# Optimization experiments

Measured on AMD Instinct MI355X. Metric: run time of the kernel, lower is better.

## Reference

```python
import jax, jax.numpy as jnp
import numpy as np

N_USERS = 100000
N_ITEMS = 50000
N_NODES = 50000
N_EDGES = 1600000
B = 16384
H, D = 4, 32  # num_heads, out_feats per head
D_IMG, D_TXT, D_AUD = 1024, 768, 128
EMB = 128
SLOPE = 0.2


def setup_inputs() -> dict:
    key = jax.random.key(0)
    ks = jax.random.split(key, 40)
    s = 0.02

    def n(i, shape, scale=s):
        return jax.random.normal(ks[i], shape, jnp.float32) * scale

    inp = {
        "user_ids": jax.random.randint(ks[0], (B,), 0, N_USERS, jnp.int32),
        "item_ids": jax.random.randint(ks[1], (B,), 0, N_ITEMS, jnp.int32),
        "src": jax.random.randint(ks[2], (N_EDGES,), 0, N_NODES, jnp.int32),
        "dst": jax.random.randint(ks[3], (N_EDGES,), 0, N_NODES, jnp.int32),
        "feat_image": jax.random.normal(ks[4], (N_NODES, D_IMG), jnp.float32),
        "feat_text": jax.random.normal(ks[5], (N_NODES, D_TXT), jnp.float32),
        "feat_audio": jax.random.normal(ks[6], (N_NODES, D_AUD), jnp.float32),
        # embedding tables
        "user_table": n(7, (N_USERS, EMB)),
        "item_table": n(8, (N_ITEMS, EMB)),
        # modality transforms (Linear: y = x @ W.T + b)
        "Wi": n(9, (32, D_IMG)), "bi": n(10, (32,)),
        "Wt": n(11, (32, D_TXT)), "bt": n(12, (32,)),
        "Wa": n(13, (32, D_AUD)), "ba": n(14, (32,)),
        # GAT params per modality: fc weight [H*D, 32], attn vectors [H, D], output bias [H*D]
        "gWi": n(15, (H * D, 32), 0.1), "ali": n(16, (H, D), 0.1), "ari": n(17, (H, D), 0.1), "gbi": n(18, (H * D,)),
        "gWt": n(19, (H * D, 32), 0.1), "alt": n(20, (H, D), 0.1), "art": n(21, (H, D), 0.1), "gbt": n(22, (H * D,)),
        "gWa": n(23, (H * D, 32), 0.1), "ala": n(24, (H, D), 0.1), "ara": n(25, (H, D), 0.1), "gba": n(26, (H * D,)),
        # final fc: Linear(32*3*H=384 -> 128)
        "fcW": n(27, (EMB, 3 * H * D)), "fcb": n(28, (EMB,)),
    }
    return inp


def _gat(x, W, al, ar, b, src, dst):
    """DGL GATConv: fc -> per-head additive attention -> edge softmax over dst -> sum."""
    h = (x @ W.T).reshape(N_NODES, H, D)                      # [N,H,D]
    el = jnp.einsum('nhd,hd->nh', h, al)                      # [N,H]
    er = jnp.einsum('nhd,hd->nh', h, ar)                      # [N,H]
    e = jax.nn.leaky_relu(el[src] + er[dst], SLOPE)           # [E,H]
    emax = jax.ops.segment_max(e, dst, num_segments=N_NODES)  # [N,H] (-inf for empty, unused)
    a = jnp.exp(e - emax[dst])                                # [E,H]
    denom = jax.ops.segment_sum(a, dst, num_segments=N_NODES)
    a = a / jnp.maximum(denom[dst], 1e-9)
    msg = a[:, :, None] * h[src]                              # [E,H,D]
    out = jax.ops.segment_sum(msg, dst, num_segments=N_NODES) # [N,H,D]
    return (out + b.reshape(1, H, D)).reshape(N_NODES, H * D)


def reference(user_ids, item_ids, src, dst, feat_image, feat_text, feat_audio,
              user_table, item_table, Wi, bi, Wt, bt, Wa, ba,
              gWi, ali, ari, gbi, gWt, alt, art, gbt, gWa, ala, ara, gba,
              fcW, fcb):
    user_emb = user_table[user_ids]
    item_emb = item_table[item_ids]
    xi = jax.nn.relu(feat_image @ Wi.T + bi)
    xt = jax.nn.relu(feat_text @ Wt.T + bt)
    xa = jax.nn.relu(feat_audio @ Wa.T + ba)
    gi = _gat(xi, gWi, ali, ari, gbi, src, dst)
    gt = _gat(xt, gWt, alt, art, gbt, src, dst)
    ga = _gat(xa, gWa, ala, ara, gba, src, dst)
    comb = jnp.concatenate([gi, gt, ga], axis=1)              # [N, 3*H*D]
    comb = jax.nn.relu(comb @ fcW.T + fcb)                    # [N, 128]
    return (user_emb, item_emb, comb)
```

## Files before the change

### kernel.cpp

```cpp
#include <hip/hip_runtime.h>
#include <stdint.h>

#define NNODES 50000
#define NEDGES 1600000
#define NB     16384
#define HD     128
#define COMBW  384
#define SCAN_BLOCKS ((NNODES + 255) / 256)

typedef unsigned short u16;
typedef __bf16 bf16x8 __attribute__((ext_vector_type(8)));
typedef float  f32x4  __attribute__((ext_vector_type(4)));

__device__ __forceinline__ float b2f(u16 u){
    union { unsigned int i; float f; } v; v.i = ((unsigned int)u) << 16; return v.f;
}
__device__ __forceinline__ u16 f2b(float f){
    union { float f; unsigned int i; } v; v.f = f;
    unsigned int x = v.i;
    unsigned int r = (x + 0x7fffu + ((x >> 16) & 1u)) >> 16;
    return (u16)r;
}
__device__ __forceinline__ bf16x8 pack8(const float* __restrict__ p){
    uint4 a = *(const uint4*)p;
    uint4 b = *(const uint4*)(p + 4);
    union { u16 s[8]; bf16x8 v; } u;
    u.s[0] = (u16)(a.x >> 16); u.s[1] = (u16)(a.y >> 16);
    u.s[2] = (u16)(a.z >> 16); u.s[3] = (u16)(a.w >> 16);
    u.s[4] = (u16)(b.x >> 16); u.s[5] = (u16)(b.y >> 16);
    u.s[6] = (u16)(b.z >> 16); u.s[7] = (u16)(b.w >> 16);
    return u.v;
}

__global__ void k_gather(const int* __restrict__ uid, const int* __restrict__ iid,
                         const float* __restrict__ utab, const float* __restrict__ itab,
                         float* __restrict__ out){
    int i = blockIdx.x * blockDim.x + threadIdx.x;
    const int total = 2 * NB * HD / 8;
    if (i >= total) return;
    int e8 = i * 8;
    const float* p;
    if (e8 < NB * HD) {
        int row = e8 >> 7, c = e8 & 127;
        p = utab + (size_t)uid[row] * HD + c;
    } else {
        int e2 = e8 - NB * HD;
        int row = e2 >> 7, c = e2 & 127;
        p = itab + (size_t)iid[row] * HD + c;
    }
    *(uint4*)(out + e8)     = *(const uint4*)p;
    *(uint4*)(out + e8 + 4) = *(const uint4*)(p + 4);
}

__global__ __launch_bounds__(256) void k_feat(const float* __restrict__ feat, int K,
                                              const float* __restrict__ W,
                                              const float* __restrict__ bias,
                                              float* __restrict__ xout){
    int wave = threadIdx.x >> 6, lane = threadIdx.x & 63;
    int quad = lane >> 4, m = lane & 15;
    int row0 = blockIdx.x * 64 + wave * 16;
    int arow = row0 + m; if (arow >= NNODES) arow = NNODES - 1;
    const float* ap  = feat + (size_t)arow * K + quad * 8;
    const float* bp0 = W + (size_t)m        * K + quad * 8;
    const float* bp1 = W + (size_t)(m + 16) * K + quad * 8;
    f32x4 c0 = {0.f,0.f,0.f,0.f}, c1 = {0.f,0.f,0.f,0.f};
    for (int k = 0; k < K; k += 32){
        bf16x8 a  = pack8(ap  + k);
        bf16x8 b0 = pack8(bp0 + k);
        bf16x8 b1 = pack8(bp1 + k);
        c0 = __builtin_amdgcn_mfma_f32_16x16x32_bf16(a, b0, c0, 0, 0, 0);
        c1 = __builtin_amdgcn_mfma_f32_16x16x32_bf16(a, b1, c1, 0, 0, 0);
    }
    float bv0 = bias[m], bv1 = bias[m + 16];
    #pragma unroll
    for (int i = 0; i < 4; i++){
        int r = row0 + quad * 4 + i;
        if (r < NNODES){
            float v0 = c0[i] + bv0; v0 = v0 > 0.f ? v0 : 0.f;
            float v1 = c1[i] + bv1; v1 = v1 > 0.f ? v1 : 0.f;
            xout[(size_t)r * 32 + m]      = v0;
            xout[(size_t)r * 32 + m + 16] = v1;
        }
    }
}

__global__ __launch_bounds__(256) void k_node(const float* __restrict__ x,
                                              const float* __restrict__ gW,
                                              const float* __restrict__ al,
                                              const float* __restrict__ ar,
                                              u16* __restrict__ hout,
                                              float* __restrict__ el,
                                              float* __restrict__ er){
    int head = blockIdx.y;
    int n = blockIdx.x * blockDim.x + threadIdx.x;
    int nc = n < NNODES ? n : NNODES - 1;
    float xr[32];
    const float4* xp = (const float4*)(x + (size_t)nc * 32);
    #pragma unroll
    for (int i = 0; i < 8; i++){
        float4 v = xp[i];
        xr[4*i] = v.x; xr[4*i+1] = v.y; xr[4*i+2] = v.z; xr[4*i+3] = v.w;
    }
    const float* wbase = gW + head * 1024;
    const float* alh = al + head * 32;
    const float* arh = ar + head * 32;
    u16* hp = hout + (size_t)nc * COMBW + head * 32;
    float elv = 0.f, erv = 0.f;
    #pragma unroll
    for (int cg = 0; cg < 4; cg++){
        float acc[8];
        #pragma unroll
        for (int c = 0; c < 8; c++){
            const float* wr = wbase + (cg * 8 + c) * 32;
            float a = 0.f;
            #pragma unroll
            for (int k = 0; k < 32; k++) a += xr[k] * wr[k];
            acc[c] = a;
            elv += a * alh[cg * 8 + c];
            erv += a * arh[cg * 8 + c];
        }
        union { u16 s[8]; uint4 q; } u;
        #pragma unroll
        for (int c = 0; c < 8; c++) u.s[c] = f2b(acc[c]);
        *(uint4*)(hp + cg * 8) = u.q;
    }
    el[(size_t)nc * 4 + head] = elv;
    er[(size_t)nc * 4 + head] = erv;
}

__global__ void k_hist(const int* __restrict__ dst, int* __restrict__ cnt){
    int i = blockIdx.x * blockDim.x + threadIdx.x;
    if (i < NEDGES) atomicAdd(&cnt[dst[i]], 1);
}

__global__ __launch_bounds__(256) void k_scan1(const int* __restrict__ cnt,
                                               int* __restrict__ rp,
                                               int* __restrict__ bsum){
    __shared__ int ws[4];
    int t = threadIdx.x, lane = t & 63, w = t >> 6;
    int i = blockIdx.x * 256 + t;
    int v = (i < NNODES) ? cnt[i] : 0;
    int x = v;
    #pragma unroll
    for (int off = 1; off < 64; off <<= 1){
        int u = __shfl_up(x, off, 64);
        if (lane >= off) x += u;
    }
    if (lane == 63) ws[w] = x;
    __syncthreads();
    if (t == 0){
        int s = 0;
        #pragma unroll
        for (int j = 0; j < 4; j++){ int tmp = ws[j]; ws[j] = s; s += tmp; }
        bsum[blockIdx.x] = s;
    }
    __syncthreads();
    if (i < NNODES) rp[i] = ws[w] + x - v;
}

__global__ __launch_bounds__(256) void k_scan2(int* __restrict__ bsum, int* __restrict__ rp){
    __shared__ int ws[4];
    int t = threadIdx.x, lane = t & 63, w = t >> 6;
    int v = (t < SCAN_BLOCKS) ? bsum[t] : 0;
    int x = v;
    #pragma unroll
    for (int off = 1; off < 64; off <<= 1){
        int u = __shfl_up(x, off, 64);
        if (lane >= off) x += u;
    }
    if (lane == 63) ws[w] = x;
    __syncthreads();
    if (t == 0){
        int s = 0;
        #pragma unroll
        for (int j = 0; j < 4; j++){ int tmp = ws[j]; ws[j] = s; s += tmp; }
        rp[NNODES] = s;
    }
    __syncthreads();
    if (t < SCAN_BLOCKS) bsum[t] = ws[w] + x - v;
}

__global__ __launch_bounds__(256) void k_scan3(int* __restrict__ rp, const int* __restrict__ bsum){
    int i = blockIdx.x * 256 + threadIdx.x;
    if (i < NNODES) rp[i] += bsum[blockIdx.x];
}

template<int WITHW>
__global__ __launch_bounds__(256) void k_scatter(const int* __restrict__ src, const int* __restrict__ dst,
                          const int* __restrict__ rp, int* __restrict__ fill,
                          int* __restrict__ col,
                          const float* __restrict__ el0, const float* __restrict__ er0,
                          const float* __restrict__ el1, const float* __restrict__ er1,
                          const float* __restrict__ el2, const float* __restrict__ er2,
                          float* __restrict__ w){
    int i = blockIdx.x * blockDim.x + threadIdx.x;
    if (i >= NEDGES) return;
    int s = src[i], d = dst[i];
    int p = rp[d] + atomicAdd(&fill[d], 1);
    col[p] = s;
    if (WITHW){
        float4 l0 = *(const float4*)(el0 + (size_t)s * 4);
        float4 r0 = *(const float4*)(er0 + (size_t)d * 4);
        float4 l1 = *(const float4*)(el1 + (size_t)s * 4);
        float4 r1 = *(const float4*)(er1 + (size_t)d * 4);
        float4 l2 = *(const float4*)(el2 + (size_t)s * 4);
        float4 r2 = *(const float4*)(er2 + (size_t)d * 4);
        float4 w0, w1, w2;
        #define LKEXP(a, b) __expf(fmaxf((a) + (b), 0.2f * ((a) + (b))))
        w0.x = LKEXP(l0.x, r0.x); w0.y = LKEXP(l0.y, r0.y); w0.z = LKEXP(l0.z, r0.z); w0.w = LKEXP(l0.w, r0.w);
        w1.x = LKEXP(l1.x, r1.x); w1.y = LKEXP(l1.y, r1.y); w1.z = LKEXP(l1.z, r1.z); w1.w = LKEXP(l1.w, r1.w);
        w2.x = LKEXP(l2.x, r2.x); w2.y = LKEXP(l2.y, r2.y); w2.z = LKEXP(l2.z, r2.z); w2.w = LKEXP(l2.w, r2.w);
        #undef LKEXP
        float4* wp = (float4*)(w + (size_t)p * 12);
        wp[0] = w0; wp[1] = w1; wp[2] = w2;
    }
}

__global__ __launch_bounds__(384) void k_gat(
        const int* __restrict__ rp, const int* __restrict__ col,
        const u16* __restrict__ hcat, const float* __restrict__ w,
        const float* __restrict__ gb0, const float* __restrict__ gb1, const float* __restrict__ gb2,
        u16* __restrict__ comb){
    int n = blockIdx.x, t = threadIdx.x;
    int mod = t >> 7;
    int head = (t >> 5) & 3;
    int beg = rp[n], end = rp[n + 1];
    float acc = 0.f, dsum = 0.f;
    const float* wp = w + (size_t)beg * 12 + mod * 4 + head;
    const u16* hbase = hcat + t;
    int e = beg;
    for (; e + 4 <= end; e += 4){
        int s0 = col[e], s1 = col[e + 1], s2 = col[e + 2], s3 = col[e + 3];
        float w0 = wp[0], w1 = wp[12], w2 = wp[24], w3 = wp[36];
        wp += 48;
        float h0 = b2f(hbase[(size_t)s0 * COMBW]);
        float h1 = b2f(hbase[(size_t)s1 * COMBW]);
        float h2 = b2f(hbase[(size_t)s2 * COMBW]);
        float h3 = b2f(hbase[(size_t)s3 * COMBW]);
        acc += w0 * h0; dsum += w0;
        acc += w1 * h1; dsum += w1;
        acc += w2 * h2; dsum += w2;
        acc += w3 * h3; dsum += w3;
    }
    for (; e < end; e++, wp += 12){
        int s = col[e];
        float wv = wp[0];
        acc += wv * b2f(hbase[(size_t)s * COMBW]);
        dsum += wv;
    }
    const float* gb = (mod == 0) ? gb0 : ((mod == 1) ? gb1 : gb2);
    comb[(size_t)n * COMBW + t] = f2b(acc / fmaxf(dsum, 1e-9f) + gb[t & 127]);
}

__global__ __launch_bounds__(128) void k_gat_fb(
        const int* __restrict__ rp, const int* __restrict__ col,
        const u16* __restrict__ hcat,
        const float* __restrict__ el0, const float* __restrict__ er0,
        const float* __restrict__ el1, const float* __restrict__ er1,
        const float* __restrict__ el2, const float* __restrict__ er2,
        const float* __restrict__ gb0, const float* __restrict__ gb1, const float* __restrict__ gb2,
        u16* __restrict__ comb){
    int n = blockIdx.x, t = threadIdx.x;
    int head = t >> 5;
    float a0 = 0.f, a1 = 0.f, a2 = 0.f, d0 = 0.f, d1 = 0.f, d2 = 0.f;
    int beg = rp[n], end = rp[n + 1];
    float e0 = er0[(size_t)n * 4 + head];
    float e1 = er1[(size_t)n * 4 + head];
    float e2 = er2[(size_t)n * 4 + head];
    for (int e = beg; e < end; e++){
        int s = col[e];
        const u16* hp = hcat + (size_t)s * COMBW + t;
        float v0 = el0[(size_t)s * 4 + head] + e0; v0 = fmaxf(v0, 0.2f * v0);
        float v1 = el1[(size_t)s * 4 + head] + e1; v1 = fmaxf(v1, 0.2f * v1);
        float v2 = el2[(size_t)s * 4 + head] + e2; v2 = fmaxf(v2, 0.2f * v2);
        float w0 = __expf(v0), w1 = __expf(v1), w2 = __expf(v2);
        a0 += w0 * b2f(hp[0]);   d0 += w0;
        a1 += w1 * b2f(hp[128]); d1 += w1;
        a2 += w2 * b2f(hp[256]); d2 += w2;
    }
    size_t o = (size_t)n * COMBW;
    comb[o + t]       = f2b(a0 / fmaxf(d0, 1e-9f) + gb0[t]);
    comb[o + 128 + t] = f2b(a1 / fmaxf(d1, 1e-9f) + gb1[t]);
    comb[o + 256 + t] = f2b(a2 / fmaxf(d2, 1e-9f) + gb2[t]);
}

__global__ __launch_bounds__(256) void k_fc(const u16* __restrict__ comb,
                                            const float* __restrict__ fcW,
                                            const float* __restrict__ fcb,
                                            float* __restrict__ out){
    int wave = threadIdx.x >> 6, lane = threadIdx.x & 63;
    int quad = lane >> 4, m = lane & 15;
    int row0 = blockIdx.x * 64 + wave * 16;
    int arow = row0 + m; if (arow >= NNODES) arow = NNODES - 1;
    const u16* ap = comb + (size_t)arow * COMBW + quad * 8;
    f32x4 c[8];
    #pragma unroll
    for (int f = 0; f < 8; f++) c[f] = (f32x4){0.f,0.f,0.f,0.f};
    for (int k = 0; k < COMBW; k += 32){
        bf16x8 a = *(const bf16x8*)(ap + k);
        #pragma unroll
        for (int f = 0; f < 8; f++){
            bf16x8 b = pack8(fcW + (size_t)(f * 16 + m) * COMBW + k + quad * 8);
            c[f] = __builtin_amdgcn_mfma_f32_16x16x32_bf16(a, b, c[f], 0, 0, 0);
        }
    }
    #pragma unroll
    for (int f = 0; f < 8; f++){
        int colc = f * 16 + m;
        float bv = fcb[colc];
        #pragma unroll
        for (int i = 0; i < 4; i++){
            int r = row0 + quad * 4 + i;
            if (r < NNODES){
                float v = c[f][i] + bv; v = v > 0.f ? v : 0.f;
                out[(size_t)(2 * NB * HD) + (size_t)r * HD + colc] = v;
            }
        }
    }
}

extern "C" void kernel_launch(void* const* d_in, const int* in_sizes, int n_in,
                              void* d_out, int out_size, void* d_ws, size_t ws_size,
                              hipStream_t stream){
    const int* uid = (const int*)d_in[0];
    const int* iid = (const int*)d_in[1];
    const int* src = (const int*)d_in[2];
    const int* dst = (const int*)d_in[3];
    const float* fimg = (const float*)d_in[4];
    const float* ftxt = (const float*)d_in[5];
    const float* faud = (const float*)d_in[6];
    const float* utab = (const float*)d_in[7];
    const float* itab = (const float*)d_in[8];
    const float* Wi = (const float*)d_in[9],  *bi = (const float*)d_in[10];
    const float* Wt = (const float*)d_in[11], *bt = (const float*)d_in[12];
    const float* Wa = (const float*)d_in[13], *ba = (const float*)d_in[14];
    const float* gWi = (const float*)d_in[15], *ali = (const float*)d_in[16],
               *ari = (const float*)d_in[17], *gbi = (const float*)d_in[18];
    const float* gWt = (const float*)d_in[19], *alt = (const float*)d_in[20],
               *art = (const float*)d_in[21], *gbt = (const float*)d_in[22];
    const float* gWa = (const float*)d_in[23], *ala = (const float*)d_in[24],
               *ara = (const float*)d_in[25], *gba = (const float*)d_in[26];
    const float* fcW = (const float*)d_in[27], *fcb = (const float*)d_in[28];
    float* out = (float*)d_out;

    char* ws = (char*)d_ws;
    u16*   hcat = (u16*)  (ws + 0);
    u16*   comb = (u16*)  (ws + 38400000);
    float* x    = (float*)(ws + 76800000);
    float* el   = (float*)(ws + 83200000);
    float* er   = (float*)(ws + 85600000);
    int*   cnt  = (int*)  (ws + 88000000);
    int*   fill = (int*)  (ws + 88200000);
    int*   rp   = (int*)  (ws + 88400000);
    int*   col  = (int*)  (ws + 88600064);
    float* w    = (float*)(ws + 95000064);
    const size_t NEED_W = 95000064u + (size_t)NEDGES * 12 * sizeof(float);
    int*   bsum = (int*)x;

    float* el0 = el,           *el1 = el + 200000, *el2 = el + 400000;
    float* er0 = er,           *er1 = er + 200000, *er2 = er + 400000;

    hipMemsetAsync(cnt, 0, 400000, stream);

    k_hist<<<(NEDGES + 255) / 256, 256, 0, stream>>>(dst, cnt);
    k_scan1<<<SCAN_BLOCKS, 256, 0, stream>>>(cnt, rp, bsum);
    k_scan2<<<1, 256, 0, stream>>>(bsum, rp);
    k_scan3<<<SCAN_BLOCKS, 256, 0, stream>>>(rp, bsum);

    k_gather<<<(2 * NB * HD / 8 + 255) / 256, 256, 0, stream>>>(uid, iid, utab, itab, out);

    dim3 ngrid((NNODES + 255) / 256, 4);
    k_feat<<<(NNODES + 63) / 64, 256, 0, stream>>>(fimg, 1024, Wi, bi, x);
    k_node<<<ngrid, 256, 0, stream>>>(x, gWi, ali, ari, hcat,       el0, er0);
    k_feat<<<(NNODES + 63) / 64, 256, 0, stream>>>(ftxt, 768, Wt, bt, x);
    k_node<<<ngrid, 256, 0, stream>>>(x, gWt, alt, art, hcat + 128, el1, er1);
    k_feat<<<(NNODES + 63) / 64, 256, 0, stream>>>(faud, 128, Wa, ba, x);
    k_node<<<ngrid, 256, 0, stream>>>(x, gWa, ala, ara, hcat + 256, el2, er2);

    if (ws_size >= NEED_W){
        k_scatter<1><<<(NEDGES + 255) / 256, 256, 0, stream>>>(src, dst, rp, fill, col,
                                                               el0, er0, el1, er1, el2, er2, w);
        k_gat<<<NNODES, 384, 0, stream>>>(rp, col, hcat, w, gbi, gbt, gba, comb);
    } else {
        k_scatter<0><<<(NEDGES + 255) / 256, 256, 0, stream>>>(src, dst, rp, fill, col,
                                                               el0, er0, el1, er1, el2, er2, w);
        k_gat_fb<<<NNODES, 128, 0, stream>>>(rp, col, hcat,
                                             el0, er0, el1, er1, el2, er2,
                                             gbi, gbt, gba, comb);
    }

    k_fc<<<(NNODES + 63) / 64, 256, 0, stream>>>(comb, fcW, fcb, out);
}
```

Baseline: 1.217 ms.

## Pre-pack weights to bf16 and restructure GAT aggregation to 128 threads per node

Adds small kernels that convert the modality and final fc weight matrices to bf16 once per call, so the MFMA loops in k_feat and k_fc load ready bf16 vectors instead of repacking fp32 weights in every block. The packed weights reuse workspace regions (comb, w) that are free at that point. k_gat now uses 128 threads per node, each handling all three modalities, to raise per-thread memory-level parallelism and cut block count overhead. The risk is lower occupancy per node and slightly different rounding, since packing truncates rather than rounds to nearest.

```diff
diff --git a/kernel.cpp b/kernel.cpp
--- a/kernel.cpp
+++ b/kernel.cpp
@@ -52,22 +52,55 @@
     *(uint4*)(out + e8 + 4) = *(const uint4*)(p + 4);
 }
 
+__global__ __launch_bounds__(256) void k_pack(const float* __restrict__ s,
+                                              u16* __restrict__ d, int n8){
+    int i = blockIdx.x * 256 + threadIdx.x;
+    if (i >= n8) return;
+    const float* p = s + (size_t)i * 8;
+    uint4 a = *(const uint4*)p, b = *(const uint4*)(p + 4);
+    union { u16 v[8]; uint4 q; } u;
+    u.v[0] = (u16)(a.x >> 16); u.v[1] = (u16)(a.y >> 16);
+    u.v[2] = (u16)(a.z >> 16); u.v[3] = (u16)(a.w >> 16);
+    u.v[4] = (u16)(b.x >> 16); u.v[5] = (u16)(b.y >> 16);
+    u.v[6] = (u16)(b.z >> 16); u.v[7] = (u16)(b.w >> 16);
+    *(uint4*)(d + (size_t)i * 8) = u.q;
+}
+
+__global__ __launch_bounds__(256) void k_pack3(const float* __restrict__ Wi,
+                                               const float* __restrict__ Wt,
+                                               const float* __restrict__ Wa,
+                                               u16* __restrict__ d){
+    int i = blockIdx.x * 256 + threadIdx.x;
+    if (i >= 7680) return;
+    const float* p;
+    if (i < 4096)       p = Wi + (size_t)i * 8;
+    else if (i < 7168)  p = Wt + (size_t)(i - 4096) * 8;
+    else                p = Wa + (size_t)(i - 7168) * 8;
+    uint4 a = *(const uint4*)p, b = *(const uint4*)(p + 4);
+    union { u16 v[8]; uint4 q; } u;
+    u.v[0] = (u16)(a.x >> 16); u.v[1] = (u16)(a.y >> 16);
+    u.v[2] = (u16)(a.z >> 16); u.v[3] = (u16)(a.w >> 16);
+    u.v[4] = (u16)(b.x >> 16); u.v[5] = (u16)(b.y >> 16);
+    u.v[6] = (u16)(b.z >> 16); u.v[7] = (u16)(b.w >> 16);
+    *(uint4*)(d + (size_t)i * 8) = u.q;
+}
+
 __global__ __launch_bounds__(256) void k_feat(const float* __restrict__ feat, int K,
-                                              const float* __restrict__ W,
+                                              const u16* __restrict__ pW,
                                               const float* __restrict__ bias,
                                               float* __restrict__ xout){
     int wave = threadIdx.x >> 6, lane = threadIdx.x & 63;
     int quad = lane >> 4, m = lane & 15;
     int row0 = blockIdx.x * 64 + wave * 16;
     int arow = row0 + m; if (arow >= NNODES) arow = NNODES - 1;
-    const float* ap  = feat + (size_t)arow * K + quad * 8;
-    const float* bp0 = W + (size_t)m        * K + quad * 8;
-    const float* bp1 = W + (size_t)(m + 16) * K + quad * 8;
+    const float* ap = feat + (size_t)arow * K + quad * 8;
+    const u16* bp0 = pW + (size_t)m        * K + quad * 8;
+    const u16* bp1 = pW + (size_t)(m + 16) * K + quad * 8;
     f32x4 c0 = {0.f,0.f,0.f,0.f}, c1 = {0.f,0.f,0.f,0.f};
     for (int k = 0; k < K; k += 32){
-        bf16x8 a  = pack8(ap  + k);
-        bf16x8 b0 = pack8(bp0 + k);
-        bf16x8 b1 = pack8(bp1 + k);
+        bf16x8 a  = pack8(ap + k);
+        bf16x8 b0 = *(const bf16x8*)(bp0 + k);
+        bf16x8 b1 = *(const bf16x8*)(bp1 + k);
         c0 = __builtin_amdgcn_mfma_f32_16x16x32_bf16(a, b0, c0, 0, 0, 0);
         c1 = __builtin_amdgcn_mfma_f32_16x16x32_bf16(a, b1, c1, 0, 0, 0);
     }
@@ -216,40 +249,47 @@
     }
 }
 
-__global__ __launch_bounds__(384) void k_gat(
+__global__ __launch_bounds__(128) void k_gat(
         const int* __restrict__ rp, const int* __restrict__ col,
         const u16* __restrict__ hcat, const float* __restrict__ w,
         const float* __restrict__ gb0, const float* __restrict__ gb1, const float* __restrict__ gb2,
         u16* __restrict__ comb){
     int n = blockIdx.x, t = threadIdx.x;
-    int mod = t >> 7;
-    int head = (t >> 5) & 3;
     int beg = rp[n], end = rp[n + 1];
-    float acc = 0.f, dsum = 0.f;
-    const float* wp = w + (size_t)beg * 12 + mod * 4 + head;
-    const u16* hbase = hcat + t;
+    float a0 = 0.f, a1 = 0.f, a2 = 0.f, d0 = 0.f, d1 = 0.f, d2 = 0.f;
+    const float* wp = w + (size_t)beg * 12 + (t >> 5);
     int e = beg;
-    for (; e + 4 <= end; e += 4){
+    for (; e + 4 <= end; e += 4, wp += 48){
         int s0 = col[e], s1 = col[e + 1], s2 = col[e + 2], s3 = col[e + 3];
-        float w0 = wp[0], w1 = wp[12], w2 = wp[24], w3 = wp[36];
-        wp += 48;
-        float h0 = b2f(hbase[(size_t)s0 * COMBW]);
-        float h1 = b2f(hbase[(size_t)s1 * COMBW]);
-        float h2 = b2f(hbase[(size_t)s2 * COMBW]);
-        float h3 = b2f(hbase[(size_t)s3 * COMBW]);
-        acc += w0 * h0; dsum += w0;
-        acc += w1 * h1; dsum += w1;
-        acc += w2 * h2; dsum += w2;
-        acc += w3 * h3; dsum += w3;
+        const u16* p0 = hcat + (size_t)s0 * COMBW + t;
+        const u16* p1 = hcat + (size_t)s1 * COMBW + t;
+        const u16* p2 = hcat + (size_t)s2 * COMBW + t;
+        const u16* p3 = hcat + (size_t)s3 * COMBW + t;
+        float w00 = wp[0],  w01 = wp[4],  w02 = wp[8];
+        float w10 = wp[12], w11 = wp[16], w12 = wp[20];
+        float w20 = wp[24], w21 = wp[28], w22 = wp[32];
+        float w30 = wp[36], w31 = wp[40], w32 = wp[44];
+        float h00 = b2f(p0[0]), h01 = b2f(p0[128]), h02 = b2f(p0[256]);
+        float h10 = b2f(p1[0]), h11 = b2f(p1[128]), h12 = b2f(p1[256]);
+        float h20 = b2f(p2[0]), h21 = b2f(p2[128]), h22 = b2f(p2[256]);
+        float h30 = b2f(p3[0]), h31 = b2f(p3[128]), h32 = b2f(p3[256]);
+        a0 += w00 * h00; d0 += w00; a1 += w01 * h01; d1 += w01; a2 += w02 * h02; d2 += w02;
+        a0 += w10 * h10; d0 += w10; a1 += w11 * h11; d1 += w11; a2 += w12 * h12; d2 += w12;
+        a0 += w20 * h20; d0 += w20; a1 += w21 * h21; d1 += w21; a2 += w22 * h22; d2 += w22;
+        a0 += w30 * h30; d0 += w30; a1 += w31 * h31; d1 += w31; a2 += w32 * h32; d2 += w32;
     }
     for (; e < end; e++, wp += 12){
         int s = col[e];
-        float wv = wp[0];
-        acc += wv * b2f(hbase[(size_t)s * COMBW]);
-        dsum += wv;
-    }
-    const float* gb = (mod == 0) ? gb0 : ((mod == 1) ? gb1 : gb2);
-    comb[(size_t)n * COMBW + t] = f2b(acc / fmaxf(dsum, 1e-9f) + gb[t & 127]);
+        const u16* hp = hcat + (size_t)s * COMBW + t;
+        float w0 = wp[0], w1 = wp[4], w2 = wp[8];
+        a0 += w0 * b2f(hp[0]);   d0 += w0;
+        a1 += w1 * b2f(hp[128]); d1 += w1;
+        a2 += w2 * b2f(hp[256]); d2 += w2;
+    }
+    size_t o = (size_t)n * COMBW;
+    comb[o + t]       = f2b(a0 / fmaxf(d0, 1e-9f) + gb0[t]);
+    comb[o + 128 + t] = f2b(a1 / fmaxf(d1, 1e-9f) + gb1[t]);
+    comb[o + 256 + t] = f2b(a2 / fmaxf(d2, 1e-9f) + gb2[t]);
 }
 
 __global__ __launch_bounds__(128) void k_gat_fb(
@@ -284,8 +324,10 @@
     comb[o + 256 + t] = f2b(a2 / fmaxf(d2, 1e-9f) + gb2[t]);
 }
 
+template<int PB>
 __global__ __launch_bounds__(256) void k_fc(const u16* __restrict__ comb,
                                             const float* __restrict__ fcW,
+                                            const u16* __restrict__ pfcW,
                                             const float* __restrict__ fcb,
                                             float* __restrict__ out){
     int wave = threadIdx.x >> 6, lane = threadIdx.x & 63;
@@ -300,7 +342,9 @@
         bf16x8 a = *(const bf16x8*)(ap + k);
         #pragma unroll
         for (int f = 0; f < 8; f++){
-            bf16x8 b = pack8(fcW + (size_t)(f * 16 + m) * COMBW + k + quad * 8);
+            bf16x8 b;
+            if (PB) b = *(const bf16x8*)(pfcW + (size_t)(f * 16 + m) * COMBW + k + quad * 8);
+            else    b = pack8(fcW + (size_t)(f * 16 + m) * COMBW + k + quad * 8);
             c[f] = __builtin_amdgcn_mfma_f32_16x16x32_bf16(a, b, c[f], 0, 0, 0);
         }
     }
@@ -356,6 +400,10 @@
     float* w    = (float*)(ws + 95000064);
     const size_t NEED_W = 95000064u + (size_t)NEDGES * 12 * sizeof(float);
     int*   bsum = (int*)x;
+    u16*   pW   = comb;
+    u16*   pWt_ = pW + 32768;
+    u16*   pWa_ = pW + 57344;
+    u16*   pfcW = (u16*)w;
 
     float* el0 = el,           *el1 = el + 200000, *el2 = el + 400000;
     float* er0 = er,           *er1 = er + 200000, *er2 = er + 400000;
@@ -367,27 +415,30 @@
     k_scan2<<<1, 256, 0, stream>>>(bsum, rp);
     k_scan3<<<SCAN_BLOCKS, 256, 0, stream>>>(rp, bsum);
 
+    k_pack3<<<30, 256, 0, stream>>>(Wi, Wt, Wa, pW);
+
     k_gather<<<(2 * NB * HD / 8 + 255) / 256, 256, 0, stream>>>(uid, iid, utab, itab, out);
 
     dim3 ngrid((NNODES + 255) / 256, 4);
-    k_feat<<<(NNODES + 63) / 64, 256, 0, stream>>>(fimg, 1024, Wi, bi, x);
+    k_feat<<<(NNODES + 63) / 64, 256, 0, stream>>>(fimg, 1024, pW,   bi, x);
     k_node<<<ngrid, 256, 0, stream>>>(x, gWi, ali, ari, hcat,       el0, er0);
-    k_feat<<<(NNODES + 63) / 64, 256, 0, stream>>>(ftxt, 768, Wt, bt, x);
+    k_feat<<<(NNODES + 63) / 64, 256, 0, stream>>>(ftxt, 768, pWt_, bt, x);
     k_node<<<ngrid, 256, 0, stream>>>(x, gWt, alt, art, hcat + 128, el1, er1);
-    k_feat<<<(NNODES + 63) / 64, 256, 0, stream>>>(faud, 128, Wa, ba, x);
+    k_feat<<<(NNODES + 63) / 64, 256, 0, stream>>>(faud, 128, pWa_, ba, x);
     k_node<<<ngrid, 256, 0, stream>>>(x, gWa, ala, ara, hcat + 256, el2, er2);
 
     if (ws_size >= NEED_W){
         k_scatter<1><<<(NEDGES + 255) / 256, 256, 0, stream>>>(src, dst, rp, fill, col,
                                                                el0, er0, el1, er1, el2, er2, w);
-        k_gat<<<NNODES, 384, 0, stream>>>(rp, col, hcat, w, gbi, gbt, gba, comb);
+        k_gat<<<NNODES, 128, 0, stream>>>(rp, col, hcat, w, gbi, gbt, gba, comb);
+        k_pack<<<24, 256, 0, stream>>>(fcW, pfcW, 6144);
+        k_fc<1><<<(NNODES + 63) / 64, 256, 0, stream>>>(comb, fcW, pfcW, fcb, out);
     } else {
         k_scatter<0><<<(NEDGES + 255) / 256, 256, 0, stream>>>(src, dst, rp, fill, col,
                                                                el0, er0, el1, er1, el2, er2, w);
         k_gat_fb<<<NNODES, 128, 0, stream>>>(rp, col, hcat,
                                              el0, er0, el1, er1, el2, er2,
                                              gbi, gbt, gba, comb);
-    }
-
-    k_fc<<<(NNODES + 63) / 64, 256, 0, stream>>>(comb, fcW, fcb, out);
-}
+        k_fc<0><<<(NNODES + 63) / 64, 256, 0, stream>>>(comb, fcW, pfcW, fcb, out);
+    }
+}
```

New measurement: 1.066 ms. -12.4%, faster.
